# Kernel tuning notes

Measured on AMD Instinct MI355X. Metric: run time of the kernel, lower is better.

The kernel has to match this reference:

```python
import jax, jax.numpy as jnp
import numpy as np

B, L, C = 16, 720, 862
RANK, K = 8, 7
EPS = 1e-5


def setup_inputs() -> dict:
    key = jax.random.key(0)
    ks = jax.random.split(key, 7)
    x = jax.random.normal(ks[0], (B, L, C), dtype=jnp.float32)
    # Conv1d(1 -> rank, k): PyTorch init ~ U(-s, s), s = 1/sqrt(in_ch*k)
    s_up = 1.0 / np.sqrt(1 * K)
    Wup = jax.random.uniform(ks[1], (RANK, 1, K), jnp.float32, -s_up, s_up)
    bup = jax.random.uniform(ks[2], (RANK,), jnp.float32, -s_up, s_up)
    # Conv1d(rank -> 1, 1)
    s_dn = 1.0 / np.sqrt(RANK * 1)
    Wdown = jax.random.uniform(ks[3], (1, RANK, 1), jnp.float32, -s_dn, s_dn)
    bdown = jax.random.uniform(ks[4], (1,), jnp.float32, -s_dn, s_dn)
    gamma = jnp.ones((C,), jnp.float32)
    beta = jnp.zeros((C,), jnp.float32)
    return {"x": x, "Wup": Wup, "bup": bup, "Wdown": Wdown,
            "bdown": bdown, "gamma": gamma, "beta": beta}


def reference(x, Wup, bup, Wdown, bdown, gamma, beta):
    b, l, c = x.shape
    h = x.reshape(b * l, 1, c)  # (N, 1, C): conv along variable dim
    pad = K // 2
    h = jax.lax.conv_general_dilated(
        h, Wup, window_strides=(1,), padding=[(pad, pad)],
        dimension_numbers=("NCH", "OIH", "NCH"))
    h = h + bup[None, :, None]                      # (N, rank, C)
    h = jax.nn.gelu(h, approximate=False)           # torch F.gelu default = erf
    # 1x1 conv down: contraction over rank channels
    h = jnp.einsum("nrc,r->nc", h, Wdown[0, :, 0]) + bdown[0]  # (N, C)
    y = x + h.reshape(b, l, c)                      # residual
    # LayerNorm over last dim (n_vars), eps=1e-5
    mu = jnp.mean(y, axis=-1, keepdims=True)
    var = jnp.mean(jnp.square(y - mu), axis=-1, keepdims=True)
    y = (y - mu) * jax.lax.rsqrt(var + EPS)
    return y * gamma + beta
```

## Files before the change

### kernel.cpp

```cpp
#include <hip/hip_runtime.h>
#include <math.h>

#define CDIM   862
#define NRANK  8
#define KW     7
#define ROWS_PER_BLOCK 4
#define THREADS (ROWS_PER_BLOCK * 64)
#define LN_EPS 1e-5f
#define NPAIRT 13
#define XH_LEN 880
#define XY_LEN 866

typedef __attribute__((ext_vector_type(8)))  short bf16x8;
typedef __attribute__((ext_vector_type(16))) float f32x16;

static __device__ __forceinline__ unsigned rne_bf16(float f) {
    const unsigned u = __float_as_uint(f);
    return (u + 0x7FFFu + ((u >> 16) & 1u)) >> 16;
}

#if __has_builtin(__builtin_amdgcn_exp2f)
#define EXP2F(x) __builtin_amdgcn_exp2f(x)
#else
#define EXP2F(x) __expf((x) * 0.69314718055994530942f)
#endif

__global__ __launch_bounds__(THREADS) void cvmc_kernel(
    const float* __restrict__ x,
    const float* __restrict__ Wup,
    const float* __restrict__ bup,
    const float* __restrict__ Wdown,
    const float* __restrict__ bdown,
    const float* __restrict__ gamma,
    const float* __restrict__ beta,
    float* __restrict__ out)
{
    const int lane = threadIdx.x & 63;
    const int wv   = threadIdx.x >> 6;
    const int row  = blockIdx.x * ROWS_PER_BLOCK + wv;

    __shared__ short sxh[ROWS_PER_BLOCK][XH_LEN];
    __shared__ float sxy[ROWS_PER_BLOCK][XY_LEN];

    const int hh    = lane >> 5;
    const int l31   = lane & 31;
    const int rbase = 4 * hh;
    float bu4[4], wd4[4];
#pragma unroll
    for (int q = 0; q < 4; ++q) {
        bu4[q] = bup[rbase + q];
        wd4[q] = Wdown[rbase + q];
    }

    bf16x8 afrag;
    {
        const bool use = (hh == 0) ? (l31 < NRANK) : (l31 >= 8 && l31 < 8 + NRANK);
        const int  rr  = (hh == 0) ? l31 : (l31 - 8);
#pragma unroll
        for (int j = 0; j < 8; ++j) {
            float wvv = (use && j < KW) ? Wup[rr * KW + j] : 0.0f;
            afrag[j] = (short)(rne_bf16(wvv) & 0xFFFFu);
        }
    }

    f32x16 cin;
#pragma unroll
    for (int i = 0; i < 16; ++i) cin[i] = 0.0f;
#pragma unroll
    for (int q = 0; q < 8; ++q) cin[q] = bu4[q & 3];

    {
        const float2* __restrict__ xr2 =
            reinterpret_cast<const float2*>(x + (size_t)row * CDIM);
        unsigned* xhW = reinterpret_cast<unsigned*>(&sxh[wv][0]);
#pragma unroll
        for (int qq = 0; qq < 7; ++qq) {
            const int i = lane + 64 * qq;
            if (i < CDIM / 2) {
                float2 v = xr2[i];
                *reinterpret_cast<float2*>(&sxy[wv][2 * i]) = v;
                xhW[2 + i] = rne_bf16(v.x) | (rne_bf16(v.y) << 16);
            }
        }
        if (lane < 2)       xhW[lane] = 0u;
        else if (lane < 9)  xhW[431 + lane] = 0u;
        else if (lane < 13) sxy[wv][862 + (lane - 9)] = 0.0f;
    }

    const float C1 = -0.0713548162f * 1.44269504088896340736f;
    const float C0 = -1.5957691216f * 1.44269504088896340736f;

    const unsigned* xhD = reinterpret_cast<const unsigned*>(&sxh[wv][0]);

    auto dp4 = [&](float t0, float t1, float t2, float t3) -> float {
        const float z0 = t0 * fmaf(t0 * t0, C1, C0);
        const float z1 = t1 * fmaf(t1 * t1, C1, C0);
        const float z2 = t2 * fmaf(t2 * t2, C1, C0);
        const float z3 = t3 * fmaf(t3 * t3, C1, C0);
        const float u0 = 1.0f + EXP2F(z0);
        const float u1 = 1.0f + EXP2F(z1);
        const float u2 = 1.0f + EXP2F(z2);
        const float u3 = 1.0f + EXP2F(z3);
        const float r01 = __builtin_amdgcn_rcpf(u0 * u1);
        const float r23 = __builtin_amdgcn_rcpf(u2 * u3);
        float n0 = (wd4[0] * t0) * u1; n0 = fmaf(wd4[1] * t1, u0, n0);
        float n1 = (wd4[2] * t2) * u3; n1 = fmaf(wd4[3] * t3, u2, n1);
        float p  = n0 * r01;
        return fmaf(n1, r23, p);
    };

    float sum = 0.0f, sumsq = 0.0f;

    for (int s = 0; s < NPAIRT; ++s) {
        const int cw = 64 * s + lane;
        const int ws = cw + 1;

        const unsigned* pw = xhD + (ws >> 1);
        const unsigned sh = (unsigned)(ws & 1) * 16u;
        const unsigned q0 = pw[0], q1 = pw[1], q2 = pw[2], q3 = pw[3], q4 = pw[4];
        union { unsigned u[4]; bf16x8 v; } bfr;
        bfr.u[0] = __builtin_amdgcn_alignbit(q1, q0, sh);
        bfr.u[1] = __builtin_amdgcn_alignbit(q2, q1, sh);
        bfr.u[2] = __builtin_amdgcn_alignbit(q3, q2, sh);
        bfr.u[3] = __builtin_amdgcn_alignbit(q4, q3, sh);

        f32x16 d = __builtin_amdgcn_mfma_f32_32x32x16_bf16(afrag, bfr.v, cin, 0, 0, 0);

        const float pA = dp4(d[0], d[1], d[2], d[3]);
        const float pB = dp4(d[4], d[5], d[6], d[7]);
        const float hA = pA + __shfl_xor(pA, 32, 64);
        const float hB = pB + __shfl_xor(pB, 32, 64);
        const float h  = (hh == 0) ? hA : hB;

        const float xv = sxy[wv][cw];
        const float y  = xv + h;
        sxy[wv][cw] = y;
        sum += y;
        sumsq = fmaf(y, y, sumsq);
    }

    {
        const int c  = 832 + l31;
        const int ws = c + 1;
        const unsigned* pw = xhD + (ws >> 1);
        const unsigned sh = (unsigned)(ws & 1) * 16u;
        const unsigned q0 = pw[0], q1 = pw[1], q2 = pw[2], q3 = pw[3], q4 = pw[4];
        union { unsigned u[4]; bf16x8 v; } bfr;
        bfr.u[0] = __builtin_amdgcn_alignbit(q1, q0, sh);
        bfr.u[1] = __builtin_amdgcn_alignbit(q2, q1, sh);
        bfr.u[2] = __builtin_amdgcn_alignbit(q3, q2, sh);
        bfr.u[3] = __builtin_amdgcn_alignbit(q4, q3, sh);

        f32x16 d = __builtin_amdgcn_mfma_f32_32x32x16_bf16(afrag, bfr.v, cin, 0, 0, 0);

        const float p = dp4(d[0], d[1], d[2], d[3]);
        const float psum = p + __shfl_xor(p, 32, 64);
        const float y = sxy[wv][c] + psum;
        if (hh == 0 && c < CDIM) {
            sxy[wv][c] = y;
            sum += y;
            sumsq = fmaf(y, y, sumsq);
        }
    }

#pragma unroll
    for (int off = 1; off < 64; off <<= 1) {
        sum   += __shfl_xor(sum, off, 64);
        sumsq += __shfl_xor(sumsq, off, 64);
    }

    const float inv  = 1.0f / (float)CDIM;
    const float mu   = sum * inv;
    const float var  = fmaf(sumsq, inv, -mu * mu);
    const float rstd = rsqrtf(var + LN_EPS);

    float2* __restrict__ yr2 = reinterpret_cast<float2*>(out + (size_t)row * CDIM);
    const float2* __restrict__ g2 = reinterpret_cast<const float2*>(gamma);
    const float2* __restrict__ b2 = reinterpret_cast<const float2*>(beta);
#pragma unroll
    for (int qq = 0; qq < 7; ++qq) {
        const int i = lane + 64 * qq;
        if (i < CDIM / 2) {
            const float2 yv = *reinterpret_cast<const float2*>(&sxy[wv][2 * i]);
            const float2 gv = g2[i];
            const float2 bv = b2[i];
            float2 o;
            o.x = fmaf((yv.x - mu) * rstd, gv.x, bv.x);
            o.y = fmaf((yv.y - mu) * rstd, gv.y, bv.y);
            yr2[i] = o;
        }
    }
}

extern "C" void kernel_launch(void* const* d_in, const int* in_sizes, int n_in,
                              void* d_out, int out_size, void* d_ws, size_t ws_size,
                              hipStream_t stream) {
    const float* x     = (const float*)d_in[0];
    const float* Wup   = (const float*)d_in[1];
    const float* bup   = (const float*)d_in[2];
    const float* Wdown = (const float*)d_in[3];
    const float* bdown = (const float*)d_in[4];
    const float* gamma = (const float*)d_in[5];
    const float* beta  = (const float*)d_in[6];
    float* out = (float*)d_out;
    (void)bdown;

    const int nrows = out_size / CDIM;
    const int nblk  = nrows / ROWS_PER_BLOCK;
    cvmc_kernel<<<nblk, THREADS, 0, stream>>>(x, Wup, bup, Wdown, bdown,
                                              gamma, beta, out);
}
```

Before: 36.99 us.

## Use all MFMA output rows by packing shifted tap copies into the A fragment

Builds the A matrix with four copies of the 8-rank filter, each shifted by zero or one tap, so each 32x32x16 MFMA yields two output positions per column instead of one. This cuts the tile loop from 13+1 iterations to 7 and drops the unaligned alignbit shuffling, since the B operand now reads aligned packed-bf16 words. In exchange each iteration does twice the GELU work, and the padded shared buffer and edge masking become more complex.

```diff
diff --git a/kernel.cpp b/kernel.cpp
--- a/kernel.cpp
+++ b/kernel.cpp
@@ -7,8 +7,8 @@
 #define ROWS_PER_BLOCK 4
 #define THREADS (ROWS_PER_BLOCK * 64)
 #define LN_EPS 1e-5f
-#define NPAIRT 13
-#define XH_LEN 880
+#define NTILE  7
+#define XH_LEN 912
 #define XY_LEN 866
 
 typedef __attribute__((ext_vector_type(8)))  short bf16x8;
@@ -54,20 +54,21 @@
 
     bf16x8 afrag;
     {
-        const bool use = (hh == 0) ? (l31 < NRANK) : (l31 >= 8 && l31 < 8 + NRANK);
-        const int  rr  = (hh == 0) ? l31 : (l31 - 8);
+        const int r    = l31 & 7;
+        const int grp  = l31 >> 3;
+        const bool use = ((grp & 1) == hh);
+        const int  sft = grp >> 1;
 #pragma unroll
         for (int j = 0; j < 8; ++j) {
-            float wvv = (use && j < KW) ? Wup[rr * KW + j] : 0.0f;
+            const int tap = j - sft;
+            float wvv = (use && tap >= 0 && tap < KW) ? Wup[r * KW + tap] : 0.0f;
             afrag[j] = (short)(rne_bf16(wvv) & 0xFFFFu);
         }
     }
 
     f32x16 cin;
 #pragma unroll
-    for (int i = 0; i < 16; ++i) cin[i] = 0.0f;
-#pragma unroll
-    for (int q = 0; q < 8; ++q) cin[q] = bu4[q & 3];
+    for (int i = 0; i < 16; ++i) cin[i] = bu4[i & 3];
 
     {
         const float2* __restrict__ xr2 =
@@ -82,9 +83,9 @@
                 xhW[2 + i] = rne_bf16(v.x) | (rne_bf16(v.y) << 16);
             }
         }
-        if (lane < 2)       xhW[lane] = 0u;
-        else if (lane < 9)  xhW[431 + lane] = 0u;
-        else if (lane < 13) sxy[wv][862 + (lane - 9)] = 0.0f;
+        if (lane < 2)        xhW[lane] = 0u;
+        else if (lane < 25)  xhW[431 + lane] = 0u;
+        else if (lane < 29)  sxy[wv][862 + (lane - 25)] = 0.0f;
     }
 
     const float C1 = -0.0713548162f * 1.44269504088896340736f;
@@ -111,53 +112,39 @@
 
     float sum = 0.0f, sumsq = 0.0f;
 
-    for (int s = 0; s < NPAIRT; ++s) {
-        const int cw = 64 * s + lane;
-        const int ws = cw + 1;
-
-        const unsigned* pw = xhD + (ws >> 1);
-        const unsigned sh = (unsigned)(ws & 1) * 16u;
-        const unsigned q0 = pw[0], q1 = pw[1], q2 = pw[2], q3 = pw[3], q4 = pw[4];
+    for (int s = 0; s < NTILE; ++s) {
+        const int w = 64 * s + lane;
         union { unsigned u[4]; bf16x8 v; } bfr;
-        bfr.u[0] = __builtin_amdgcn_alignbit(q1, q0, sh);
-        bfr.u[1] = __builtin_amdgcn_alignbit(q2, q1, sh);
-        bfr.u[2] = __builtin_amdgcn_alignbit(q3, q2, sh);
-        bfr.u[3] = __builtin_amdgcn_alignbit(q4, q3, sh);
+        bfr.u[0] = xhD[w];
+        bfr.u[1] = xhD[w + 1];
+        bfr.u[2] = xhD[w + 2];
+        bfr.u[3] = xhD[w + 3];
 
         f32x16 d = __builtin_amdgcn_mfma_f32_32x32x16_bf16(afrag, bfr.v, cin, 0, 0, 0);
 
-        const float pA = dp4(d[0], d[1], d[2], d[3]);
-        const float pB = dp4(d[4], d[5], d[6], d[7]);
-        const float hA = pA + __shfl_xor(pA, 32, 64);
-        const float hB = pB + __shfl_xor(pB, 32, 64);
-        const float h  = (hh == 0) ? hA : hB;
+        const float pE0 = dp4(d[0],  d[1],  d[2],  d[3]);
+        const float pE2 = dp4(d[4],  d[5],  d[6],  d[7]);
+        const float pE1 = dp4(d[8],  d[9],  d[10], d[11]);
+        const float pE3 = dp4(d[12], d[13], d[14], d[15]);
 
-        const float xv = sxy[wv][cw];
-        const float y  = xv + h;
-        sxy[wv][cw] = y;
-        sum += y;
-        sumsq = fmaf(y, y, sumsq);
-    }
+        const float hE0 = pE0 + __shfl_xor(pE0, 32, 64);
+        const float hE2 = pE2 + __shfl_xor(pE2, 32, 64);
+        const float hE1 = pE1 + __shfl_xor(pE1, 32, 64);
+        const float hE3 = pE3 + __shfl_xor(pE3, 32, 64);
 
-    {
-        const int c  = 832 + l31;
-        const int ws = c + 1;
-        const unsigned* pw = xhD + (ws >> 1);
-        const unsigned sh = (unsigned)(ws & 1) * 16u;
-        const unsigned q0 = pw[0], q1 = pw[1], q2 = pw[2], q3 = pw[3], q4 = pw[4];
-        union { unsigned u[4]; bf16x8 v; } bfr;
-        bfr.u[0] = __builtin_amdgcn_alignbit(q1, q0, sh);
-        bfr.u[1] = __builtin_amdgcn_alignbit(q2, q1, sh);
-        bfr.u[2] = __builtin_amdgcn_alignbit(q3, q2, sh);
-        bfr.u[3] = __builtin_amdgcn_alignbit(q4, q3, sh);
+        const int   eS = 128 * s + 2 * l31 - 1 + 64 * hh;
+        const float h0 = hh ? hE2 : hE0;
+        const float h1 = hh ? hE3 : hE1;
 
-        f32x16 d = __builtin_amdgcn_mfma_f32_32x32x16_bf16(afrag, bfr.v, cin, 0, 0, 0);
-
-        const float p = dp4(d[0], d[1], d[2], d[3]);
-        const float psum = p + __shfl_xor(p, 32, 64);
-        const float y = sxy[wv][c] + psum;
-        if (hh == 0 && c < CDIM) {
-            sxy[wv][c] = y;
+        if ((unsigned)eS < CDIM) {
+            const float y = sxy[wv][eS] + h0;
+            sxy[wv][eS] = y;
+            sum += y;
+            sumsq = fmaf(y, y, sumsq);
+        }
+        if ((unsigned)(eS + 1) < CDIM) {
+            const float y = sxy[wv][eS + 1] + h1;
+            sxy[wv][eS + 1] = y;
             sum += y;
             sumsq = fmaf(y, y, sumsq);
         }
```

After: 36.02 us. -2.6%, faster.
